# Kernel tuning notes

Hardware: AMD Instinct MI355X
Metric: run time of the kernel (lower is better)

Reference implementation:

```python
import jax, jax.numpy as jnp
import numpy as np

B, T, D, H = 8, 512, 1024, 16
DK = D // H  # 64
EPS = 1e-3  # Keras BatchNormalization default epsilon


def batchnorm(x, gamma, beta):
    # Keras BN over feature axis (-1), training-mode batch statistics over (B, T)
    mean = jnp.mean(x, axis=(0, 1), keepdims=True)
    var = jnp.var(x, axis=(0, 1), keepdims=True)
    return (x - mean) * jax.lax.rsqrt(var + EPS) * gamma + beta


def setup_inputs() -> dict:
    key = jax.random.key(0)
    ks = jax.random.split(key, 12)
    s = 0.05
    return {
        "x": jax.random.normal(ks[0], (B, T, D), dtype=jnp.float32),
        "Wq": jax.random.uniform(ks[1], (H, D, DK), dtype=jnp.float32, minval=-s, maxval=s),
        "Wk": jax.random.uniform(ks[2], (H, D, DK), dtype=jnp.float32, minval=-s, maxval=s),
        "Wv": jax.random.uniform(ks[3], (H, D, DK), dtype=jnp.float32, minval=-s, maxval=s),
        "W": jax.random.uniform(ks[4], (D, D), dtype=jnp.float32, minval=-s, maxval=s),
        "W1": jax.random.normal(ks[5], (D, D), dtype=jnp.float32) * 0.02,
        "b1": jnp.zeros((D,), dtype=jnp.float32),
        "W2": jax.random.normal(ks[6], (D, D), dtype=jnp.float32) * 0.02,
        "b2": jnp.zeros((D,), dtype=jnp.float32),
        "g1": jnp.ones((D,), dtype=jnp.float32),
        "be1": jnp.zeros((D,), dtype=jnp.float32),
        "g2": jnp.ones((D,), dtype=jnp.float32),
        "be2": jnp.zeros((D,), dtype=jnp.float32),
    }


def reference(x, Wq, Wk, Wv, W, W1, b1, W2, b2, g1, be1, g2, be2):
    # Batched multi-head attention (replaces the per-head Python loop)
    q = jnp.einsum("btd,hdk->bhtk", x, Wq)
    k = jnp.einsum("btd,hdk->bhtk", x, Wk)
    v = jnp.einsum("btd,hdk->bhtk", x, Wv)
    scores = jnp.einsum("bhtk,bhsk->bhts", q, k) / jnp.sqrt(jnp.float32(DK))
    w = jax.nn.softmax(scores, axis=-1)
    attn = jnp.einsum("bhts,bhsk->bhtk", w, v)
    # concat heads: [B,H,T,DK] -> [B,T,H*DK] (head-major concat order as in the loop)
    concat = jnp.transpose(attn, (0, 2, 1, 3)).reshape(B, T, D)
    out = concat @ W
    out1 = batchnorm(x + out, g1, be1)
    out2 = jax.nn.relu(out1 @ W1 + b1) @ W2 + b2
    return batchnorm(out1 + out2, g2, be2)
```

## Files before the change

### kernel.cpp

```cpp
#include <hip/hip_runtime.h>
#include <hip/hip_bf16.h>
#include <cstdint>

#define Bn 8
#define Tn 512
#define Dn 1024
#define Hn 16
#define DKn 64
#define Mn (Bn * Tn)

typedef unsigned short u16;
typedef short bf16x8 __attribute__((ext_vector_type(8)));
typedef float f32x4 __attribute__((ext_vector_type(4)));

__device__ __forceinline__ u16 f2bf(float f) {
  unsigned int u = __builtin_bit_cast(unsigned int, f);
  u += 0x7fffu + ((u >> 16) & 1u);
  return (u16)(u >> 16);
}
__device__ __forceinline__ unsigned int pack2bf(float lo, float hi) {
  return (unsigned int)f2bf(lo) | ((unsigned int)f2bf(hi) << 16);
}

__device__ __forceinline__ void gl2lds16(const void* g, void* l) {
  __builtin_amdgcn_global_load_lds(
      (const __attribute__((address_space(1))) unsigned int*)g,
      (__attribute__((address_space(3))) unsigned int*)l,
      16, 0, 0);
}

__device__ __forceinline__ void hard_barrier() {
  __builtin_amdgcn_sched_barrier(0);
  __builtin_amdgcn_s_barrier();
  __builtin_amdgcn_sched_barrier(0);
}
#define WAITV(n_) asm volatile("s_waitcnt vmcnt(" #n_ ")" ::: "memory")

__global__ __launch_bounds__(256) void prep_k(
    const float* __restrict__ x, u16* __restrict__ xb,
    const float* __restrict__ wq, const float* __restrict__ wk,
    const float* __restrict__ wv, u16* __restrict__ wqkvT,
    const float* __restrict__ W, const float* __restrict__ W1,
    const float* __restrict__ W2, u16* __restrict__ wt,
    u16* __restrict__ w1t, u16* __restrict__ w2t)
{
  const int bid = blockIdx.x;
  const int t = threadIdx.x;
  if (bid < 2048) {
    const size_t i = ((size_t)bid * 256 + t) * 8;
    float4 a = *reinterpret_cast<const float4*>(&x[i]);
    float4 b = *reinterpret_cast<const float4*>(&x[i + 4]);
    uint4 w;
    w.x = pack2bf(a.x, a.y); w.y = pack2bf(a.z, a.w);
    w.z = pack2bf(b.x, b.y); w.w = pack2bf(b.z, b.w);
    *reinterpret_cast<uint4*>(&xb[i]) = w;
  } else if (bid < 2816) {
    const int idx = bid - 2048;
    const int kt = idx & 15;
    const int y  = idx >> 4;
    const int tau = y >> 4, head = y & 15;
    const float* src = (tau == 0 ? wq : tau == 1 ? wk : wv) + (size_t)head * 65536;
    const int n  = t & 63;
    const int kq = (t >> 6) << 4;
    const int k0 = kt << 6;
    u16 v[16];
#pragma unroll
    for (int j = 0; j < 16; j++)
      v[j] = f2bf(src[(size_t)(k0 + kq + j) * 64 + n]);
    u16* d = &wqkvT[((size_t)tau * 1024 + head * 64 + n) * 1024 + k0 + kq];
    *reinterpret_cast<uint4*>(&d[0]) = *reinterpret_cast<uint4*>(&v[0]);
    *reinterpret_cast<uint4*>(&d[8]) = *reinterpret_cast<uint4*>(&v[8]);
  } else {
    const int idx = bid - 2816;
    const int kt = idx & 15;
    const int rest = idx >> 4;
    const int ntl = rest & 15, z = rest >> 4;
    const float* src = (z == 0 ? W : z == 1 ? W1 : W2);
    u16* dst = (z == 0 ? wt : z == 1 ? w1t : w2t);
    const int n  = (ntl << 6) + (t & 63);
    const int kq = (t >> 6) << 4;
    const int k0 = kt << 6;
    u16 v[16];
#pragma unroll
    for (int j = 0; j < 16; j++)
      v[j] = f2bf(src[(size_t)(k0 + kq + j) * 1024 + n]);
    u16* d = &dst[(size_t)n * 1024 + k0 + kq];
    *reinterpret_cast<uint4*>(&d[0]) = *reinterpret_cast<uint4*>(&v[0]);
    *reinterpret_cast<uint4*>(&d[8]) = *reinterpret_cast<uint4*>(&v[8]);
  }
}

template<int VT>
__global__ __launch_bounds__(512) void mgemm_k(
    const u16* __restrict__ A, const u16* __restrict__ Bt,
    u16* __restrict__ Cb, int ldc, u16* __restrict__ Vt)
{
  __shared__ __align__(16) u16 As[3][4096];
  __shared__ __align__(16) u16 Bs[3][4096];

  const int nwg = gridDim.x * gridDim.y;
  const int fid = blockIdx.y * gridDim.x + blockIdx.x;
  const int lid = (fid & 7) * (nwg >> 3) + (fid >> 3);
  const int bx = lid % gridDim.x, by = lid / gridDim.x;

  const int tid  = threadIdx.x;
  const int lane = tid & 63;
  const int wid  = tid >> 6;
  const int wm = wid >> 2, wn = wid & 3;
  const int g4 = lane >> 4, r15 = lane & 15;
  const int m0 = by << 7, n0 = bx << 7;

  const int srow  = tid >> 2;
  const int sslot = tid & 3;
  const int ssw   = (srow ^ (srow >> 2)) & 3;
  const int sk8   = ((sslot ^ ssw) << 3);
  const u16* ga0 = &A[(size_t)(m0 + srow) * 1024 + sk8];
  const u16* gb0 = &Bt[(size_t)(n0 + srow) * 1024 + sk8];
  const int lofs = wid * 1024;

  f32x4 acc[4][2] = {};

  auto stage_t = [&](int t, int buf) {
    gl2lds16(ga0 + t * 32, (char*)As[buf] + lofs);
    gl2lds16(gb0 + t * 32, (char*)Bs[buf] + lofs);
  };
  auto compute_t = [&](int buf) {
    bf16x8 af[4], bfr[2];
#pragma unroll
    for (int m = 0; m < 4; m++) {
      int row = wm * 64 + m * 16 + r15;
      int sw = (row ^ (row >> 2)) & 3;
      af[m] = *reinterpret_cast<const bf16x8*>(
          (const char*)As[buf] + row * 64 + ((g4 ^ sw) << 4));
    }
#pragma unroll
    for (int n = 0; n < 2; n++) {
      int row = wn * 32 + n * 16 + r15;
      int sw = (row ^ (row >> 2)) & 3;
      bfr[n] = *reinterpret_cast<const bf16x8*>(
          (const char*)Bs[buf] + row * 64 + ((g4 ^ sw) << 4));
    }
#pragma unroll
    for (int m = 0; m < 4; m++)
#pragma unroll
      for (int n = 0; n < 2; n++)
        acc[m][n] = __builtin_amdgcn_mfma_f32_16x16x32_bf16(af[m], bfr[n], acc[m][n], 0, 0, 0);
  };

  stage_t(0, 0);
  stage_t(1, 1);

  int rd = 0, wr = 2;
#pragma unroll 1
  for (int t = 0; t < 30; ++t) {
    stage_t(t + 2, wr);
    WAITV(4);
    hard_barrier();
    compute_t(rd);
    hard_barrier();
    wr = rd;
    rd = (rd + 1 == 3) ? 0 : rd + 1;
  }
  WAITV(2);
  hard_barrier();
  compute_t(0);
  hard_barrier();
  WAITV(0);
  hard_barrier();
  compute_t(1);

  if (VT && bx >= 16) {
    const int vcol0 = n0 - 2048;
#pragma unroll
    for (int m = 0; m < 4; m++) {
      int row0 = m0 + wm * 64 + m * 16 + g4 * 4;
      int bI = row0 >> 9, s = row0 & 511;
#pragma unroll
      for (int n = 0; n < 2; n++) {
        int cv = vcol0 + wn * 32 + n * 16 + r15;
        int hh = cv >> 6, dk = cv & 63;
        uint2 pk;
        pk.x = pack2bf(acc[m][n][0], acc[m][n][1]);
        pk.y = pack2bf(acc[m][n][2], acc[m][n][3]);
        *reinterpret_cast<uint2*>(
            &Vt[(((size_t)(bI * 16 + hh) * 64 + dk) << 9) + s]) = pk;
      }
    }
    return;
  }

#pragma unroll
  for (int m = 0; m < 4; m++) {
    int row = m0 + wm * 64 + m * 16 + g4 * 4;
#pragma unroll
    for (int n = 0; n < 2; n++) {
      int col = n0 + wn * 32 + n * 16 + r15;
#pragma unroll
      for (int j = 0; j < 4; j++)
        Cb[(size_t)(row + j) * ldc + col] = f2bf(acc[m][n][j]);
    }
  }
}

template<int BIAS, int RELU, int OUTM, int RES, int RESNORM>
__global__ __launch_bounds__(512) void mgemm64_k(
    const u16* __restrict__ A, const u16* __restrict__ Bt,
    const float* __restrict__ bias, u16* __restrict__ Cb,
    const float* __restrict__ Rres, float* __restrict__ Rout,
    float* __restrict__ psum, float* __restrict__ psumsq,
    const float* __restrict__ nsc, const float* __restrict__ nsh)
{
  __shared__ __align__(16) u16 As[3][2048];
  __shared__ __align__(16) u16 Bs[3][4096];

  const int nwg = gridDim.x * gridDim.y;
  const int fid = blockIdx.y * gridDim.x + blockIdx.x;
  const int lid = (fid & 7) * (nwg >> 3) + (fid >> 3);
  const int bx = lid % gridDim.x, by = lid / gridDim.x;

  const int tid  = threadIdx.x;
  const int lane = tid & 63;
  const int wid  = tid >> 6;
  const int wm = wid >> 2, wn = wid & 3;
  const int g4 = lane >> 4, r15 = lane & 15;
  const int m0 = by << 6, n0 = bx << 7;

  const int srow  = lane >> 2;
  const int sslot = lane & 3;
  const int arow  = (wid & 3) * 16 + srow;
  const int asw   = (arow ^ (arow >> 2)) & 3;
  const u16* gaP  = &A[(size_t)(m0 + arow) * 1024 + ((sslot ^ asw) << 3)];
  const int brow  = wid * 16 + srow;
  const int bsw   = (brow ^ (brow >> 2)) & 3;
  const u16* gbP  = &Bt[(size_t)(n0 + brow) * 1024 + ((sslot ^ bsw) << 3)];

  f32x4 acc[2][2] = {};

  auto stage_t = [&](int t, int buf) {
    if (wid < 4)
      gl2lds16(gaP + t * 32, (char*)As[buf] + (wid & 3) * 1024);
    gl2lds16(gbP + t * 32, (char*)Bs[buf] + wid * 1024);
  };
  auto compute_t = [&](int buf) {
    bf16x8 af[2], bfr[2];
#pragma unroll
    for (int m = 0; m < 2; m++) {
      int row = wm * 32 + m * 16 + r15;
      int sw = (row ^ (row >> 2)) & 3;
      af[m] = *reinterpret_cast<const bf16x8*>(
          (const char*)As[buf] + row * 64 + ((g4 ^ sw) << 4));
    }
#pragma unroll
    for (int n = 0; n < 2; n++) {
      int row = wn * 32 + n * 16 + r15;
      int sw = (row ^ (row >> 2)) & 3;
      bfr[n] = *reinterpret_cast<const bf16x8*>(
          (const char*)Bs[buf] + row * 64 + ((g4 ^ sw) << 4));
    }
#pragma unroll
    for (int m = 0; m < 2; m++)
#pragma unroll
      for (int n = 0; n < 2; n++)
        acc[m][n] = __builtin_amdgcn_mfma_f32_16x16x32_bf16(af[m], bfr[n], acc[m][n], 0, 0, 0);
  };

  stage_t(0, 0);
  stage_t(1, 1);

  int rd = 0, wr = 2;
#pragma unroll 1
  for (int t = 0; t < 30; ++t) {
    stage_t(t + 2, wr);
    if (wid < 4) { WAITV(4); } else { WAITV(2); }
    hard_barrier();
    compute_t(rd);
    hard_barrier();
    wr = rd;
    rd = (rd + 1 == 3) ? 0 : rd + 1;
  }
  if (wid < 4) { WAITV(2); } else { WAITV(1); }
  hard_barrier();
  compute_t(0);
  hard_barrier();
  WAITV(0);
  hard_barrier();
  compute_t(1);

  float bb[2] = {0.f, 0.f};
  if (BIAS) {
#pragma unroll
    for (int n = 0; n < 2; n++) bb[n] = bias[n0 + wn * 32 + n * 16 + r15];
  }

  if (RES) {
    float sc_[2], sh_[2];
    if (RESNORM) {
#pragma unroll
      for (int n = 0; n < 2; n++) {
        int col = n0 + wn * 32 + n * 16 + r15;
        sc_[n] = nsc[col];
        sh_[n] = nsh[col];
      }
    }
    float sp[2] = {0.f, 0.f}, sq[2] = {0.f, 0.f};
#pragma unroll
    for (int m = 0; m < 2; m++) {
      int row = m0 + wm * 32 + m * 16 + g4 * 4;
#pragma unroll
      for (int n = 0; n < 2; n++) {
        int col = n0 + wn * 32 + n * 16 + r15;
#pragma unroll
        for (int j = 0; j < 4; j++) {
          float v = acc[m][n][j] + bb[n];
          float res = Rres[(size_t)(row + j) * 1024 + col];
          if (RESNORM) res = fmaf(res, sc_[n], sh_[n]);
          float r = v + res;
          Rout[(size_t)(row + j) * 1024 + col] = r;
          sp[n] += r;
          sq[n] = fmaf(r, r, sq[n]);
        }
      }
    }
#pragma unroll
    for (int n = 0; n < 2; n++) {
      sp[n] += __shfl_xor(sp[n], 16, 64);
      sp[n] += __shfl_xor(sp[n], 32, 64);
      sq[n] += __shfl_xor(sq[n], 16, 64);
      sq[n] += __shfl_xor(sq[n], 32, 64);
    }
    if (g4 == 0) {
      int slot = (by << 1) + wm;
#pragma unroll
      for (int n = 0; n < 2; n++) {
        int col = n0 + wn * 32 + n * 16 + r15;
        psum[(size_t)slot * 1024 + col] = sp[n];
        psumsq[(size_t)slot * 1024 + col] = sq[n];
      }
    }
    return;
  }

#pragma unroll
  for (int m = 0; m < 2; m++) {
    int row = m0 + wm * 32 + m * 16 + g4 * 4;
#pragma unroll
    for (int n = 0; n < 2; n++) {
      int col = n0 + wn * 32 + n * 16 + r15;
#pragma unroll
      for (int j = 0; j < 4; j++) {
        float v = acc[m][n][j];
        if (BIAS) v += bb[n];
        if (RELU) v = fmaxf(v, 0.f);
        if (OUTM == 1) Cb[(size_t)(row + j) * 1024 + col] = f2bf(v);
      }
    }
  }
}

__global__ __launch_bounds__(256, 2) void attn_k(
    const u16* __restrict__ qk, const u16* __restrict__ Vt,
    u16* __restrict__ o)
{
  __shared__ __align__(16) unsigned char Ks[2][16384];
  __shared__ __align__(16) unsigned char Vs[2][16384];
  __shared__ __align__(16) unsigned char Ps[16384];

  const int bh  = blockIdx.x;
  const int qc  = blockIdx.y;
  const int b   = bh >> 4, h = bh & 15;
  const int tid = threadIdx.x;
  const int lane = tid & 63;
  const int wv   = tid >> 6;
  const int qcol = lane & 15;
  const int g    = lane >> 4;

  const size_t rowbase = (size_t)b * Tn;
  const size_t qrow0   = rowbase + qc * 64 + wv * 16;

  bf16x8 qf[2];
  {
    const u16* qp = &qk[(qrow0 + qcol) * 2048 + h * 64 + g * 8];
    qf[0] = *reinterpret_cast<const bf16x8*>(qp);
    qf[1] = *reinterpret_cast<const bf16x8*>(qp + 32);
  }

  f32x4 oa[4] = {};
  float m_run = -3e38f, l_run = 0.f;

  const int krow = tid >> 3, kch = tid & 7;
  const int vrow = tid >> 4, vch = tid & 15;
  unsigned char* Pw = &Ps[wv * 4096];

  auto stage_kv = [&](int c, int buf) {
#pragma unroll
    for (int i = 0; i < 4; i++) {
      int row = i * 32 + krow;
      const u16* gk = &qk[(rowbase + c * 128 + row) * 2048 + 1024 + h * 64
                          + ((kch ^ (row & 7)) << 3)];
      gl2lds16(gk, (char*)Ks[buf] + wv * 1024 + i * 4096);
    }
#pragma unroll
    for (int i = 0; i < 4; i++) {
      int row = i * 16 + vrow;
      const u16* gv = &Vt[(((size_t)bh * 64 + row) << 9) + c * 128
                          + ((vch ^ (row & 7)) << 3)];
      gl2lds16(gv, (char*)Vs[buf] + wv * 1024 + i * 4096);
    }
  };

  auto compute_c = [&](int cur) {
    f32x4 sf[8];
#pragma unroll
    for (int t = 0; t < 8; t++) {
      sf[t] = (f32x4){0.f, 0.f, 0.f, 0.f};
      const int srow = t * 16 + qcol;
      const int base = srow * 128;
      const int sw = srow & 7;
#pragma unroll
      for (int ks = 0; ks < 2; ks++) {
        bf16x8 a = *reinterpret_cast<const bf16x8*>(
            &Ks[cur][base + (((ks * 4 + g) ^ sw) << 4)]);
        sf[t] = __builtin_amdgcn_mfma_f32_16x16x32_bf16(a, qf[ks], sf[t], 0, 0, 0);
      }
    }

    float mc = -3e38f;
#pragma unroll
    for (int t = 0; t < 8; t++)
#pragma unroll
      for (int r = 0; r < 4; r++) {
        float s = sf[t][r] * 0.125f;
        sf[t][r] = s;
        mc = fmaxf(mc, s);
      }
    mc = fmaxf(mc, __shfl_xor(mc, 16, 64));
    mc = fmaxf(mc, __shfl_xor(mc, 32, 64));
    float mnew = fmaxf(m_run, mc);
    float alpha = __expf(m_run - mnew);
    m_run = mnew;

    float lsum = 0.f;
#pragma unroll
    for (int t = 0; t < 8; t++)
#pragma unroll
      for (int r = 0; r < 4; r++) {
        float e = __expf(sf[t][r] - mnew);
        sf[t][r] = e;
        lsum += e;
      }
    lsum += __shfl_xor(lsum, 16, 64);
    lsum += __shfl_xor(lsum, 32, 64);
    l_run = l_run * alpha + lsum;

#pragma unroll
    for (int j = 0; j < 4; j++) {
      float av = __shfl(alpha, (g << 4) + g * 4 + j, 64);
#pragma unroll
      for (int nt = 0; nt < 4; nt++) oa[nt][j] *= av;
    }

#pragma unroll
    for (int t = 0; t < 8; t++) {
      int o0 = t * 32 + g * 8;
      int chunk = o0 >> 4;
      int sb = ((chunk ^ (qcol & 7)) << 4) | (o0 & 15);
      *reinterpret_cast<unsigned int*>(&Pw[qcol * 256 + sb]) =
          pack2bf(sf[t][0], sf[t][1]);
      *reinterpret_cast<unsigned int*>(&Pw[qcol * 256 + sb + 4]) =
          pack2bf(sf[t][2], sf[t][3]);
    }

    bf16x8 pa[4];
#pragma unroll
    for (int ks = 0; ks < 4; ks++)
      pa[ks] = *reinterpret_cast<const bf16x8*>(
          &Pw[qcol * 256 + (((ks * 4 + g) ^ (qcol & 7)) << 4)]);
#pragma unroll
    for (int nt = 0; nt < 4; nt++) {
      const int vr = nt * 16 + qcol;
      const int vsw = vr & 7;
#pragma unroll
      for (int ks = 0; ks < 4; ks++) {
        bf16x8 bvf = *reinterpret_cast<const bf16x8*>(
            &Vs[cur][vr * 256 + (((ks * 4 + g) ^ vsw) << 4)]);
        oa[nt] = __builtin_amdgcn_mfma_f32_16x16x32_bf16(pa[ks], bvf, oa[nt], 0, 0, 0);
      }
    }
  };

  stage_kv(0, 0);
#pragma unroll 1
  for (int c = 0; c < 3; ++c) {
    stage_kv(c + 1, (c + 1) & 1);
    WAITV(8);
    hard_barrier();
    compute_c(c & 1);
    hard_barrier();
  }
  WAITV(0);
  hard_barrier();
  compute_c(1);

  float rl = 1.f / l_run;
#pragma unroll
  for (int j = 0; j < 4; j++) {
    float il = __shfl(rl, (g << 4) + g * 4 + j, 64);
#pragma unroll
    for (int nt = 0; nt < 4; nt++)
      o[(qrow0 + g * 4 + j) * 1024 + h * 64 + nt * 16 + qcol] =
          f2bf(oa[nt][j] * il);
  }
}

__global__ __launch_bounds__(256) void reduce_stats_k(
    const float* __restrict__ ps, const float* __restrict__ pq,
    const float* __restrict__ g, const float* __restrict__ be,
    float* __restrict__ scale, float* __restrict__ shift)
{
  const int col = blockIdx.x * 256 + threadIdx.x;
  float s = 0.f, q = 0.f;
  for (int p = 0; p < 128; p++) {
    s += ps[(size_t)p * Dn + col];
    q += pq[(size_t)p * Dn + col];
  }
  const float invn = 1.f / 4096.f;
  float mean = s * invn;
  float var = q * invn - mean * mean;
  float inv = rsqrtf(var + 1e-3f);
  float sc = g[col] * inv;
  scale[col] = sc;
  shift[col] = be[col] - mean * sc;
}

template<int OUTMODE>
__global__ __launch_bounds__(256) void norm_k(
    const float* __restrict__ r, const float* __restrict__ scale,
    const float* __restrict__ shift, float* __restrict__ o, u16* __restrict__ ob)
{
  const size_t idx = (size_t)blockIdx.x * 256 + threadIdx.x;
  const int c4 = ((int)idx & 255) << 2;
  float4 rv = *reinterpret_cast<const float4*>(&r[idx << 2]);
  float4 sc = *reinterpret_cast<const float4*>(&scale[c4]);
  float4 sh = *reinterpret_cast<const float4*>(&shift[c4]);
  float4 ov = make_float4(fmaf(rv.x, sc.x, sh.x), fmaf(rv.y, sc.y, sh.y),
                          fmaf(rv.z, sc.z, sh.z), fmaf(rv.w, sc.w, sh.w));
  if (OUTMODE == 0) {
    *reinterpret_cast<float4*>(&o[idx << 2]) = ov;
  } else {
    uint2 p;
    p.x = pack2bf(ov.x, ov.y);
    p.y = pack2bf(ov.z, ov.w);
    *reinterpret_cast<uint2*>(&ob[idx << 2]) = p;
  }
}

extern "C" void kernel_launch(void* const* d_in, const int* in_sizes, int n_in,
                              void* d_out, int out_size, void* d_ws, size_t ws_size,
                              hipStream_t stream)
{
  const float* x   = (const float*)d_in[0];
  const float* wq  = (const float*)d_in[1];
  const float* wk  = (const float*)d_in[2];
  const float* wv  = (const float*)d_in[3];
  const float* W   = (const float*)d_in[4];
  const float* W1  = (const float*)d_in[5];
  const float* b1  = (const float*)d_in[6];
  const float* W2  = (const float*)d_in[7];
  const float* b2  = (const float*)d_in[8];
  const float* g1  = (const float*)d_in[9];
  const float* be1 = (const float*)d_in[10];
  const float* g2  = (const float*)d_in[11];
  const float* be2 = (const float*)d_in[12];

  float* out = (float*)d_out;
  float* ws  = (float*)d_ws;

  const size_t NB = (size_t)Mn * Dn;
  float* ws1    = ws;
  float* ws2    = ws1 + NB;
  float* psum   = ws2 + NB;
  float* psumsq = psum + 128 * Dn;
  float* scale1 = psumsq + 128 * Dn;
  float* shift1 = scale1 + Dn;
  float* scale2 = shift1 + Dn;
  float* shift2 = scale2 + Dn;
  u16* xb      = (u16*)(shift2 + Dn);
  u16* qkb     = xb + NB;
  u16* vtb     = qkb + 2 * NB;
  u16* concatb = vtb + NB;
  u16* wqkvT   = concatb + NB;
  u16* wt      = wqkvT + 3 * 1048576;
  u16* w1t     = wt + 1048576;
  u16* w2t     = w1t + 1048576;
  u16* out1b = qkb;
  u16* hb    = qkb + NB;

  dim3 b256(256), b512(512);

  prep_k<<<dim3(3584), b256, 0, stream>>>(x, xb, wq, wk, wv, wqkvT,
                                          W, W1, W2, wt, w1t, w2t);
  mgemm_k<1><<<dim3(24, 32), b512, 0, stream>>>(xb, wqkvT, qkb, 2048, vtb);
  attn_k<<<dim3(128, 8), b256, 0, stream>>>(qkb, vtb, concatb);
  mgemm64_k<0, 0, 2, 1, 0><<<dim3(8, 64), b512, 0, stream>>>(
      concatb, wt, nullptr, nullptr, x, ws1, psum, psumsq, nullptr, nullptr);
  reduce_stats_k<<<dim3(4), b256, 0, stream>>>(psum, psumsq, g1, be1, scale1, shift1);
  norm_k<2><<<dim3(NB / 1024), b256, 0, stream>>>(ws1, scale1, shift1, nullptr, out1b);
  mgemm64_k<1, 1, 1, 0, 0><<<dim3(8, 64), b512, 0, stream>>>(
      out1b, w1t, b1, hb, nullptr, nullptr, nullptr, nullptr, nullptr, nullptr);
  mgemm64_k<1, 0, 2, 1, 1><<<dim3(8, 64), b512, 0, stream>>>(
      hb, w2t, b2, nullptr, ws1, ws2, psum, psumsq, scale1, shift1);
  reduce_stats_k<<<dim3(4), b256, 0, stream>>>(psum, psumsq, g2, be2, scale2, shift2);
  norm_k<0><<<dim3(NB / 1024), b256, 0, stream>>>(ws2, scale2, shift2, out, nullptr);
}
```

Before: 175.8 us.

## Store pre-norm residual intermediates in bf16 and relax barrier scheduling fences

The pre-batchnorm residual buffers ws1/ws2 are now written and read as bf16 instead of fp32. This halves their traffic in the GEMM epilogues and both normalization kernels, and norm_k now processes 8 elements per thread. Batch statistics are still accumulated from the fp32 values, but the normalized outputs are computed from rounded bf16 residuals, which adds precision loss to the final output. The sched_barrier fences around s_barrier are replaced by plain memory clobbers, which lets the compiler schedule more freely around barriers.

```diff
diff --git a/kernel.cpp b/kernel.cpp
--- a/kernel.cpp
+++ b/kernel.cpp
@@ -18,6 +18,9 @@
   u += 0x7fffu + ((u >> 16) & 1u);
   return (u16)(u >> 16);
 }
+__device__ __forceinline__ float bf2f(u16 v) {
+  return __builtin_bit_cast(float, (unsigned int)v << 16);
+}
 __device__ __forceinline__ unsigned int pack2bf(float lo, float hi) {
   return (unsigned int)f2bf(lo) | ((unsigned int)f2bf(hi) << 16);
 }
@@ -29,10 +32,10 @@
       16, 0, 0);
 }
 
-__device__ __forceinline__ void hard_barrier() {
-  __builtin_amdgcn_sched_barrier(0);
+__device__ __forceinline__ void bar() {
+  asm volatile("" ::: "memory");
   __builtin_amdgcn_s_barrier();
-  __builtin_amdgcn_sched_barrier(0);
+  asm volatile("" ::: "memory");
 }
 #define WAITV(n_) asm volatile("s_waitcnt vmcnt(" #n_ ")" ::: "memory")
 
@@ -155,18 +158,18 @@
   for (int t = 0; t < 30; ++t) {
     stage_t(t + 2, wr);
     WAITV(4);
-    hard_barrier();
+    bar();
     compute_t(rd);
-    hard_barrier();
+    bar();
     wr = rd;
     rd = (rd + 1 == 3) ? 0 : rd + 1;
   }
   WAITV(2);
-  hard_barrier();
+  bar();
   compute_t(0);
-  hard_barrier();
+  bar();
   WAITV(0);
-  hard_barrier();
+  bar();
   compute_t(1);
 
   if (VT && bx >= 16) {
@@ -206,7 +209,8 @@
 __global__ __launch_bounds__(512) void mgemm64_k(
     const u16* __restrict__ A, const u16* __restrict__ Bt,
     const float* __restrict__ bias, u16* __restrict__ Cb,
-    const float* __restrict__ Rres, float* __restrict__ Rout,
+    const float* __restrict__ RresF, const u16* __restrict__ RresB,
+    u16* __restrict__ Rout,
     float* __restrict__ psum, float* __restrict__ psumsq,
     const float* __restrict__ nsc, const float* __restrict__ nsh)
 {
@@ -272,18 +276,18 @@
   for (int t = 0; t < 30; ++t) {
     stage_t(t + 2, wr);
     if (wid < 4) { WAITV(4); } else { WAITV(2); }
-    hard_barrier();
+    bar();
     compute_t(rd);
-    hard_barrier();
+    bar();
     wr = rd;
     rd = (rd + 1 == 3) ? 0 : rd + 1;
   }
   if (wid < 4) { WAITV(2); } else { WAITV(1); }
-  hard_barrier();
+  bar();
   compute_t(0);
-  hard_barrier();
+  bar();
   WAITV(0);
-  hard_barrier();
+  bar();
   compute_t(1);
 
   float bb[2] = {0.f, 0.f};
@@ -311,11 +315,13 @@
         int col = n0 + wn * 32 + n * 16 + r15;
 #pragma unroll
         for (int j = 0; j < 4; j++) {
+          size_t off = (size_t)(row + j) * 1024 + col;
           float v = acc[m][n][j] + bb[n];
-          float res = Rres[(size_t)(row + j) * 1024 + col];
-          if (RESNORM) res = fmaf(res, sc_[n], sh_[n]);
+          float res;
+          if (RESNORM) res = fmaf(bf2f(RresB[off]), sc_[n], sh_[n]);
+          else         res = RresF[off];
           float r = v + res;
-          Rout[(size_t)(row + j) * 1024 + col] = r;
+          Rout[off] = f2bf(r);
           sp[n] += r;
           sq[n] = fmaf(r, r, sq[n]);
         }
@@ -493,12 +499,12 @@
   for (int c = 0; c < 3; ++c) {
     stage_kv(c + 1, (c + 1) & 1);
     WAITV(8);
-    hard_barrier();
+    bar();
     compute_c(c & 1);
-    hard_barrier();
+    bar();
   }
   WAITV(0);
-  hard_barrier();
+  bar();
   compute_c(1);
 
   float rl = 1.f / l_run;
@@ -534,23 +540,33 @@
 
 template<int OUTMODE>
 __global__ __launch_bounds__(256) void norm_k(
-    const float* __restrict__ r, const float* __restrict__ scale,
+    const u16* __restrict__ r, const float* __restrict__ scale,
     const float* __restrict__ shift, float* __restrict__ o, u16* __restrict__ ob)
 {
-  const size_t idx = (size_t)blockIdx.x * 256 + threadIdx.x;
-  const int c4 = ((int)idx & 255) << 2;
-  float4 rv = *reinterpret_cast<const float4*>(&r[idx << 2]);
-  float4 sc = *reinterpret_cast<const float4*>(&scale[c4]);
-  float4 sh = *reinterpret_cast<const float4*>(&shift[c4]);
-  float4 ov = make_float4(fmaf(rv.x, sc.x, sh.x), fmaf(rv.y, sc.y, sh.y),
-                          fmaf(rv.z, sc.z, sh.z), fmaf(rv.w, sc.w, sh.w));
+  const size_t i8 = ((size_t)blockIdx.x * 256 + threadIdx.x) * 8;
+  const int col = (int)(i8 & 1023);
+  uint4 rv = *reinterpret_cast<const uint4*>(&r[i8]);
+  const u16* rs = reinterpret_cast<const u16*>(&rv);
+  float4 sc0 = *reinterpret_cast<const float4*>(&scale[col]);
+  float4 sc1 = *reinterpret_cast<const float4*>(&scale[col + 4]);
+  float4 sh0 = *reinterpret_cast<const float4*>(&shift[col]);
+  float4 sh1 = *reinterpret_cast<const float4*>(&shift[col + 4]);
+  const float scs[8] = {sc0.x, sc0.y, sc0.z, sc0.w, sc1.x, sc1.y, sc1.z, sc1.w};
+  const float shs[8] = {sh0.x, sh0.y, sh0.z, sh0.w, sh1.x, sh1.y, sh1.z, sh1.w};
+  float v[8];
+#pragma unroll
+  for (int j = 0; j < 8; j++)
+    v[j] = fmaf(bf2f(rs[j]), scs[j], shs[j]);
   if (OUTMODE == 0) {
-    *reinterpret_cast<float4*>(&o[idx << 2]) = ov;
+    float4 o0 = make_float4(v[0], v[1], v[2], v[3]);
+    float4 o1 = make_float4(v[4], v[5], v[6], v[7]);
+    *reinterpret_cast<float4*>(&o[i8]) = o0;
+    *reinterpret_cast<float4*>(&o[i8 + 4]) = o1;
   } else {
-    uint2 p;
-    p.x = pack2bf(ov.x, ov.y);
-    p.y = pack2bf(ov.z, ov.w);
-    *reinterpret_cast<uint2*>(&ob[idx << 2]) = p;
+    uint4 p;
+    p.x = pack2bf(v[0], v[1]); p.y = pack2bf(v[2], v[3]);
+    p.z = pack2bf(v[4], v[5]); p.w = pack2bf(v[6], v[7]);
+    *reinterpret_cast<uint4*>(&ob[i8]) = p;
   }
 }
 
@@ -576,15 +592,15 @@
   float* ws  = (float*)d_ws;
 
   const size_t NB = (size_t)Mn * Dn;
-  float* ws1    = ws;
-  float* ws2    = ws1 + NB;
-  float* psum   = ws2 + NB;
+  float* psum   = ws;
   float* psumsq = psum + 128 * Dn;
   float* scale1 = psumsq + 128 * Dn;
   float* shift1 = scale1 + Dn;
   float* scale2 = shift1 + Dn;
   float* shift2 = scale2 + Dn;
-  u16* xb      = (u16*)(shift2 + Dn);
+  u16* ws1b    = (u16*)(shift2 + Dn);
+  u16* ws2b    = ws1b + NB;
+  u16* xb      = ws2b + NB;
   u16* qkb     = xb + NB;
   u16* vtb     = qkb + 2 * NB;
   u16* concatb = vtb + NB;
@@ -602,13 +618,16 @@
   mgemm_k<1><<<dim3(24, 32), b512, 0, stream>>>(xb, wqkvT, qkb, 2048, vtb);
   attn_k<<<dim3(128, 8), b256, 0, stream>>>(qkb, vtb, concatb);
   mgemm64_k<0, 0, 2, 1, 0><<<dim3(8, 64), b512, 0, stream>>>(
-      concatb, wt, nullptr, nullptr, x, ws1, psum, psumsq, nullptr, nullptr);
+      concatb, wt, nullptr, nullptr, x, nullptr, ws1b, psum, psumsq,
+      nullptr, nullptr);
   reduce_stats_k<<<dim3(4), b256, 0, stream>>>(psum, psumsq, g1, be1, scale1, shift1);
-  norm_k<2><<<dim3(NB / 1024), b256, 0, stream>>>(ws1, scale1, shift1, nullptr, out1b);
+  norm_k<2><<<dim3(2048), b256, 0, stream>>>(ws1b, scale1, shift1, nullptr, out1b);
   mgemm64_k<1, 1, 1, 0, 0><<<dim3(8, 64), b512, 0, stream>>>(
-      out1b, w1t, b1, hb, nullptr, nullptr, nullptr, nullptr, nullptr, nullptr);
+      out1b, w1t, b1, hb, nullptr, nullptr, nullptr, nullptr, nullptr,
+      nullptr, nullptr);
   mgemm64_k<1, 0, 2, 1, 1><<<dim3(8, 64), b512, 0, stream>>>(
-      hb, w2t, b2, nullptr, ws1, ws2, psum, psumsq, scale1, shift1);
+      hb, w2t, b2, nullptr, nullptr, ws1b, ws2b, psum, psumsq,
+      scale1, shift1);
   reduce_stats_k<<<dim3(4), b256, 0, stream>>>(psum, psumsq, g2, be2, scale2, shift2);
-  norm_k<0><<<dim3(NB / 1024), b256, 0, stream>>>(ws2, scale2, shift2, out, nullptr);
-}
+  norm_k<0><<<dim3(2048), b256, 0, stream>>>(ws2b, scale2, shift2, out, nullptr);
+}
```

After: 171.4 us. 1.03x faster.
